# Kernel optimization log

Measured on AMD Instinct MI355X. Metric: run time of the kernel, lower is better.

The kernel has to match this reference:

```python
import jax, jax.numpy as jnp
import numpy as np

D = 1024
H = 16
HD = D // H  # 64
FF = 4 * D
EPS = 1e-5


def _xavier(key, shape):
    fan_in, fan_out = shape[1], shape[0]
    limit = float(np.sqrt(6.0 / (fan_in + fan_out)))
    return jax.random.uniform(key, shape, jnp.float32, -limit, limit)


def setup_inputs() -> dict:
    key = jax.random.key(0)
    ks = jax.random.split(key, 8)
    x = jax.random.normal(ks[0], (2, 2048, D), jnp.float32)
    return {
        "x": x,
        "w_qkv": _xavier(ks[1], (3 * D, D)),
        "b_qkv": jnp.zeros((3 * D,), jnp.float32),
        "w_out": _xavier(ks[2], (D, D)),
        "b_out": jnp.zeros((D,), jnp.float32),
        "w1": _xavier(ks[3], (FF, D)),
        "b1": jnp.zeros((FF,), jnp.float32),
        "w2": _xavier(ks[4], (D, FF)),
        "b2": jnp.zeros((D,), jnp.float32),
        "ln1_g": jnp.ones((D,), jnp.float32),
        "ln1_b": jnp.zeros((D,), jnp.float32),
        "ln2_g": jnp.ones((D,), jnp.float32),
        "ln2_b": jnp.zeros((D,), jnp.float32),
    }


def _layernorm(x, g, b):
    mu = jnp.mean(x, -1, keepdims=True)
    var = jnp.mean(jnp.square(x - mu), -1, keepdims=True)
    return (x - mu) * jax.lax.rsqrt(var + EPS) * g + b


def reference(x, w_qkv, b_qkv, w_out, b_out, w1, b1, w2, b2,
              ln1_g, ln1_b, ln2_g, ln2_b):
    B, S, _ = x.shape
    # pre-LN attention branch
    h = _layernorm(x, ln1_g, ln1_b)
    qkv = h @ w_qkv.T + b_qkv                      # [B,S,3D]
    qkv = qkv.reshape(B, S, H, 3 * HD).transpose(0, 2, 1, 3)  # [B,H,S,3hd]
    q, k, v = jnp.split(qkv, 3, axis=-1)
    scores = jnp.einsum('bhqd,bhkd->bhqk', q, k) / np.sqrt(HD)
    attn = jax.nn.softmax(scores, axis=-1)
    ctx = jnp.einsum('bhqk,bhkd->bhqd', attn, v)   # [B,H,S,hd]
    ctx = ctx.transpose(0, 2, 1, 3).reshape(B, S, D)
    x = x + (ctx @ w_out.T + b_out)
    # pre-LN MLP branch
    h = _layernorm(x, ln2_g, ln2_b)
    h = jax.nn.relu(h @ w1.T + b1)
    x = x + (h @ w2.T + b2)
    return x
```

## Files before the change

kernel.cpp:

```cpp
#include <hip/hip_runtime.h>
#include <hip/hip_bf16.h>

typedef __attribute__((ext_vector_type(8))) short bf16x8;
typedef __attribute__((ext_vector_type(4))) float f32x4;
typedef __attribute__((ext_vector_type(16))) float f32x16;
typedef __attribute__((ext_vector_type(4))) unsigned short u16x4;
typedef __attribute__((ext_vector_type(4))) unsigned int u32x4;
typedef unsigned short u16;

__device__ __forceinline__ u16 f2bf(float f) {
  unsigned u = __builtin_bit_cast(unsigned, f);
  u += 0x7fffu + ((u >> 16) & 1u);
  return (u16)(u >> 16);
}
__device__ __forceinline__ float bf2f(u16 u) {
  unsigned v = ((unsigned)u) << 16;
  return __builtin_bit_cast(float, v);
}
__device__ __forceinline__ unsigned cvt_pk_bf16(float lo, float hi) {
  unsigned r;
  asm("v_cvt_pk_bf16_f32 %0, %1, %2" : "=v"(r) : "v"(lo), "v"(hi));
  return r;
}
__device__ __forceinline__ float exp2_fast(float x) {
  float r;
  asm("v_exp_f32 %0, %1" : "=v"(r) : "v"(x));
  return r;
}

__device__ __forceinline__ void gl_lds16(const void* g, void* l) {
  __builtin_amdgcn_global_load_lds((const __attribute__((address_space(1))) void*)g,
                                   (__attribute__((address_space(3))) void*)l,
                                   16, 0, 0);
}

__device__ __forceinline__ void bar() {
  asm volatile("" ::: "memory");
  __builtin_amdgcn_s_barrier();
  asm volatile("" ::: "memory");
}

__global__ __launch_bounds__(256) void ln_cvt(const float* __restrict__ x,
                                              const float* __restrict__ g,
                                              const float* __restrict__ b,
                                              u16* __restrict__ out,
                                              const float* __restrict__ wa,
                                              const float* __restrict__ wb,
                                              const float* __restrict__ wc,
                                              const float* __restrict__ wd,
                                              u16* __restrict__ oa,
                                              u16* __restrict__ ob,
                                              u16* __restrict__ oc,
                                              u16* __restrict__ od) {
  __shared__ float red[8];
  const int t = threadIdx.x;
  if (blockIdx.x < 4096) {
    const int row = blockIdx.x;
    const int lane = t & 63, w = t >> 6;
    const float4 v = ((const float4*)(x + (size_t)row * 1024))[t];
    float s = v.x + v.y + v.z + v.w;
    float q = v.x * v.x + v.y * v.y + v.z * v.z + v.w * v.w;
#pragma unroll
    for (int off = 32; off; off >>= 1) {
      s += __shfl_down(s, off);
      q += __shfl_down(q, off);
    }
    if (lane == 0) { red[w] = s; red[4 + w] = q; }
    __syncthreads();
    s = red[0] + red[1] + red[2] + red[3];
    q = red[4] + red[5] + red[6] + red[7];
    const float mu = s * (1.f / 1024.f);
    const float var = q * (1.f / 1024.f) - mu * mu;
    const float rs = rsqrtf(var + 1e-5f);
    const float4 gv = ((const float4*)g)[t];
    const float4 bv = ((const float4*)b)[t];
    u16x4 o;
    o.x = f2bf((v.x - mu) * rs * gv.x + bv.x);
    o.y = f2bf((v.y - mu) * rs * gv.y + bv.y);
    o.z = f2bf((v.z - mu) * rs * gv.z + bv.z);
    o.w = f2bf((v.w - mu) * rs * gv.w + bv.w);
    ((u16x4*)(out + (size_t)row * 1024))[t] = o;
  } else {
    int i = (blockIdx.x - 4096) * 256 + t;
    const int stride = 2048 * 256;
    for (; i < 3145728; i += stride) {
      const float* src;
      u16* dst;
      int j;
      if (i < 786432) { src = wa; dst = oa; j = i; }
      else if (i < 1048576) { src = wb; dst = ob; j = i - 786432; }
      else if (i < 2097152) { src = wc; dst = oc; j = i - 1048576; }
      else { src = wd; dst = od; j = i - 2097152; }
      float4 v = ((const float4*)src)[j];
      u16x4 o;
      o.x = f2bf(v.x); o.y = f2bf(v.y); o.z = f2bf(v.z); o.w = f2bf(v.w);
      ((u16x4*)dst)[j] = o;
    }
  }
}

__global__ __launch_bounds__(256) void ln_k(const float* __restrict__ x,
                                            const float* __restrict__ g,
                                            const float* __restrict__ b,
                                            u16* __restrict__ out) {
  const int row = blockIdx.x;
  const int t = threadIdx.x;
  const int lane = t & 63, w = t >> 6;
  const float4 v = ((const float4*)(x + (size_t)row * 1024))[t];
  float s = v.x + v.y + v.z + v.w;
  float q = v.x * v.x + v.y * v.y + v.z * v.z + v.w * v.w;
#pragma unroll
  for (int off = 32; off; off >>= 1) {
    s += __shfl_down(s, off);
    q += __shfl_down(q, off);
  }
  __shared__ float red[8];
  if (lane == 0) { red[w] = s; red[4 + w] = q; }
  __syncthreads();
  s = red[0] + red[1] + red[2] + red[3];
  q = red[4] + red[5] + red[6] + red[7];
  const float mu = s * (1.f / 1024.f);
  const float var = q * (1.f / 1024.f) - mu * mu;
  const float rs = rsqrtf(var + 1e-5f);
  const float4 gv = ((const float4*)g)[t];
  const float4 bv = ((const float4*)b)[t];
  u16x4 o;
  o.x = f2bf((v.x - mu) * rs * gv.x + bv.x);
  o.y = f2bf((v.y - mu) * rs * gv.y + bv.y);
  o.z = f2bf((v.z - mu) * rs * gv.z + bv.z);
  o.w = f2bf((v.w - mu) * rs * gv.w + bv.w);
  ((u16x4*)(out + (size_t)row * 1024))[t] = o;
}

template <int EPI>
__global__ __launch_bounds__(512, 2) void gemm8(const u16* __restrict__ A,
                                                const u16* __restrict__ B,
                                                const float* __restrict__ bias,
                                                void* __restrict__ outp,
                                                const int N, const int K) {
  __shared__ u16 lds[65536];
  const int t = threadIdx.x;
  const int lane = t & 63, w = t >> 6;
  const int wm = w >> 2, wn = w & 3;
  const int l15 = lane & 15, lhi = lane >> 4;
  const int nbx = gridDim.x;
  const int nwg = nbx * gridDim.y;
  const int orig = blockIdx.y * nbx + blockIdx.x;
  const int cpx = nwg >> 3;
  const int lid = (orig & 7) * cpx + (orig >> 3);
  const long bm = (long)(lid / nbx) * 256, bn = (long)(lid % nbx) * 256;
  const u16* Ab = A + bm * K;
  const u16* Bb = B + bn * K;
  const int nt = K >> 6;
  const int ni2 = nt >> 1;

  const int srow0 = t >> 3, sg0 = (t & 7) ^ (srow0 & 7);
  const int srow1 = 64 + srow0, sg1 = (t & 7) ^ (srow1 & 7);

#define STAGE8(Mb, hf, kt_, dstb)                                             \
  do {                                                                        \
    const long kk_ = (long)(kt_) << 6;                                        \
    gl_lds16(Mb + (size_t)((hf) * 128 + srow0) * K + kk_ + sg0 * 8,           \
             &lds[(dstb) + w * 512]);                                         \
    gl_lds16(Mb + (size_t)((hf) * 128 + srow1) * K + kk_ + sg1 * 8,           \
             &lds[(dstb) + 4096 + w * 512]);                                  \
  } while (0)

#define LOADA(db, mi, fk0, fk1)                                               \
  {                                                                           \
    const int r_ = (mi) * 16 + l15;                                           \
    const int b_ = ((db) * 2 + wm) * 8192 + r_ * 64;                          \
    fk0 = *(const bf16x8*)&lds[b_ + ((lhi ^ (r_ & 7)) << 3)];                 \
    fk1 = *(const bf16x8*)&lds[b_ + (((4 + lhi) ^ (r_ & 7)) << 3)];           \
  }

#define LOADB(db)                                                             \
  _Pragma("unroll")                                                           \
  for (int ni = 0; ni < 4; ++ni) {                                            \
    const int R_ = wn * 64 + ni * 16 + l15;                                   \
    const int b_ = 32768 + ((db) * 2 + (R_ >> 7)) * 8192 + (R_ & 127) * 64;   \
    bq[ni][0] = *(const bf16x8*)&lds[b_ + ((lhi ^ (R_ & 7)) << 3)];           \
    bq[ni][1] = *(const bf16x8*)&lds[b_ + (((4 + lhi) ^ (R_ & 7)) << 3)];     \
  }

#define MM(q, a0k0, a0k1, a1k0, a1k1)                                         \
  __builtin_amdgcn_s_setprio(1);                                              \
  _Pragma("unroll")                                                           \
  for (int ni = 0; ni < 4; ++ni) {                                            \
    acc[2 * (q)][ni] = __builtin_amdgcn_mfma_f32_16x16x32_bf16(               \
        a0k0, bq[ni][0], acc[2 * (q)][ni], 0, 0, 0);                          \
    acc[2 * (q)][ni] = __builtin_amdgcn_mfma_f32_16x16x32_bf16(               \
        a0k1, bq[ni][1], acc[2 * (q)][ni], 0, 0, 0);                          \
    acc[2 * (q) + 1][ni] = __builtin_amdgcn_mfma_f32_16x16x32_bf16(           \
        a1k0, bq[ni][0], acc[2 * (q) + 1][ni], 0, 0, 0);                      \
    acc[2 * (q) + 1][ni] = __builtin_amdgcn_mfma_f32_16x16x32_bf16(           \
        a1k1, bq[ni][1], acc[2 * (q) + 1][ni], 0, 0, 0);                      \
  }                                                                           \
  __builtin_amdgcn_s_setprio(0);

  f32x4 acc[8][4] = {};
  STAGE8(Bb, 0, 0, 32768 + 0);
  STAGE8(Bb, 1, 0, 32768 + 8192);
  STAGE8(Ab, 0, 0, 0);
  STAGE8(Ab, 1, 0, 8192);
  STAGE8(Bb, 0, 1, 32768 + 16384);
  STAGE8(Bb, 1, 1, 32768 + 24576);
  asm volatile("s_waitcnt vmcnt(4)" ::: "memory");
  bar();

  for (int it = 0; it < ni2; ++it) {
    const int t0 = 2 * it, t1 = 2 * it + 1;
    const bool sN = (it + 1) < ni2;
    bf16x8 bq[4][2];
    bf16x8 a0, a1, a2, a3;
    LOADA(0, 0, a0, a1) LOADA(0, 1, a2, a3) LOADB(0);
    STAGE8(Ab, 0, t1, 16384);
    bar();
    MM(0, a0, a1, a2, a3)
    bar();
    LOADA(0, 2, a0, a1) LOADA(0, 3, a2, a3)
    STAGE8(Ab, 1, t1, 24576);
    if (sN) STAGE8(Bb, 0, t0 + 2, 32768 + 0);
    bar();
    MM(1, a0, a1, a2, a3)
    bar();
    LOADA(0, 4, a0, a1) LOADA(0, 5, a2, a3)
    if (sN) STAGE8(Bb, 1, t0 + 2, 32768 + 8192);
    bar();
    MM(2, a0, a1, a2, a3)
    bar();
    LOADA(0, 6, a0, a1) LOADA(0, 7, a2, a3)
    if (sN) asm volatile("s_waitcnt vmcnt(4)" ::: "memory");
    else    asm volatile("s_waitcnt vmcnt(0)" ::: "memory");
    bar();
    MM(3, a0, a1, a2, a3)
    bar();
    LOADA(1, 0, a0, a1) LOADA(1, 1, a2, a3) LOADB(1);
    if (sN) STAGE8(Ab, 0, t0 + 2, 0);
    bar();
    MM(0, a0, a1, a2, a3)
    bar();
    LOADA(1, 2, a0, a1) LOADA(1, 3, a2, a3)
    if (sN) {
      STAGE8(Ab, 1, t0 + 2, 8192);
      STAGE8(Bb, 0, t1 + 2, 32768 + 16384);
    }
    bar();
    MM(1, a0, a1, a2, a3)
    bar();
    LOADA(1, 4, a0, a1) LOADA(1, 5, a2, a3)
    if (sN) STAGE8(Bb, 1, t1 + 2, 32768 + 24576);
    bar();
    MM(2, a0, a1, a2, a3)
    bar();
    LOADA(1, 6, a0, a1) LOADA(1, 7, a2, a3)
    if (sN) asm volatile("s_waitcnt vmcnt(4)" ::: "memory");
    else    asm volatile("s_waitcnt vmcnt(0)" ::: "memory");
    bar();
    MM(3, a0, a1, a2, a3)
    bar();
  }
#undef STAGE8
#undef LOADA
#undef LOADB
#undef MM
#pragma unroll
  for (int ni = 0; ni < 4; ++ni) {
    const long col = bn + wn * 64 + ni * 16 + l15;
    const float bj = bias[col];
#pragma unroll
    for (int mi = 0; mi < 8; ++mi) {
      const long row0 = bm + wm * 128 + mi * 16 + lhi * 4;
#pragma unroll
      for (int r = 0; r < 4; ++r) {
        const float v = acc[mi][ni][r] + bj;
        const long idx = (row0 + r) * N + col;
        if constexpr (EPI == 0) {
          ((u16*)outp)[idx] = f2bf(v);
        } else {
          ((u16*)outp)[idx] = f2bf(v > 0.f ? v : 0.f);
        }
      }
    }
  }
}

template <int BM, int BN, int BK, int TH, int WN, int MR, int NR, int EPI>
__global__ __launch_bounds__(TH, 2) void gemm_rot(const u16* __restrict__ A,
                                                  const u16* __restrict__ B,
                                                  const float* __restrict__ bias,
                                                  const float* __restrict__ res,
                                                  void* __restrict__ outp,
                                                  const int N, const int K) {
  constexpr int GPR = BK / 8;
  constexpr int KS = BK / 32;
  constexpr int AELEMS = BM * BK;
  constexpr int BELEMS = BN * BK;
  constexpr int NC = (BM + BN) * GPR / TH;
  static_assert((BM * GPR) % TH == 0 && ((BM + BN) * GPR) % TH == 0, "");
  __shared__ u16 lds[3][AELEMS + BELEMS];
  const int t = threadIdx.x;
  const int lane = t & 63, w = t >> 6;
  const int wm = w / WN, wn = w % WN;
  const int l15 = lane & 15, lhi = lane >> 4;
  const int nbx = gridDim.x;
  const int nwg = nbx * gridDim.y;
  const int orig = blockIdx.y * nbx + blockIdx.x;
  const int cpx = nwg >> 3;
  const int lid = (orig & 7) * cpx + (orig >> 3);
  const long bm = (long)(lid / nbx) * BM, bn = (long)(lid % nbx) * BN;
  const u16* Ab = A + bm * K;
  const u16* Bb = B + bn * K;
  const int nk = K / BK;

#define STAGE(kt_, bufi)                                                      \
  do {                                                                        \
    const long kk_ = (long)(kt_) * BK;                                        \
    _Pragma("unroll")                                                         \
    for (int j = 0; j < NC; ++j) {                                            \
      const int sj = j * TH + t;                                              \
      const u16* src_;                                                        \
      if ((j + 1) * TH <= BM * GPR) {                                         \
        const int row_ = sj / GPR, grp_ = sj % GPR;                           \
        const int g_ = (BK == 32) ? (grp_ ^ ((row_ >> 1) & 3))                \
                                  : (grp_ ^ (row_ & 7));                      \
        src_ = Ab + (size_t)row_ * K + kk_ + g_ * 8;                          \
      } else {                                                                \
        const int sb_ = sj - BM * GPR;                                        \
        const int row_ = sb_ / GPR, grp_ = sb_ % GPR;                         \
        const int g_ = (BK == 32) ? (grp_ ^ ((row_ >> 1) & 3))                \
                                  : (grp_ ^ (row_ & 7));                      \
        src_ = Bb + (size_t)row_ * K + kk_ + g_ * 8;                          \
      }                                                                       \
      gl_lds16(src_, &lds[bufi][(size_t)(j * TH + w * 64) * 8]);              \
    }                                                                         \
  } while (0)

  f32x4 acc[MR][NR] = {};
  STAGE(0, 0);
  STAGE(1, 1);
  for (int i = 0; i < nk; ++i) {
    if (i + 1 < nk) {
      if constexpr (NC == 3)      asm volatile("s_waitcnt vmcnt(3)" ::: "memory");
      else if constexpr (NC == 4) asm volatile("s_waitcnt vmcnt(4)" ::: "memory");
      else                        asm volatile("s_waitcnt vmcnt(6)" ::: "memory");
    } else {
      asm volatile("s_waitcnt vmcnt(0)" ::: "memory");
    }
    bar();
    if (i + 2 < nk) STAGE(i + 2, (i + 2) % 3);
    const u16* bufA = lds[i % 3];
    const u16* bufB = bufA + AELEMS;
    bf16x8 av[MR][KS], bv[NR][KS];
#pragma unroll
    for (int ii = 0; ii < MR; ++ii) {
      const int R = wm * (MR * 16) + ii * 16 + l15;
#pragma unroll
      for (int ks = 0; ks < KS; ++ks) {
        const int pos = (BK == 32) ? (lhi ^ ((R >> 1) & 3))
                                   : ((ks * 4 + lhi) ^ (R & 7));
        av[ii][ks] = *(const bf16x8*)&bufA[R * BK + (pos << 3)];
      }
    }
#pragma unroll
    for (int jj = 0; jj < NR; ++jj) {
      const int R = wn * (NR * 16) + jj * 16 + l15;
#pragma unroll
      for (int ks = 0; ks < KS; ++ks) {
        const int pos = (BK == 32) ? (lhi ^ ((R >> 1) & 3))
                                   : ((ks * 4 + lhi) ^ (R & 7));
        bv[jj][ks] = *(const bf16x8*)&bufB[R * BK + (pos << 3)];
      }
    }
    __builtin_amdgcn_s_setprio(1);
#pragma unroll
    for (int ii = 0; ii < MR; ++ii)
#pragma unroll
      for (int jj = 0; jj < NR; ++jj)
#pragma unroll
        for (int ks = 0; ks < KS; ++ks)
          acc[ii][jj] = __builtin_amdgcn_mfma_f32_16x16x32_bf16(av[ii][ks], bv[jj][ks],
                                                                acc[ii][jj], 0, 0, 0);
    __builtin_amdgcn_s_setprio(0);
  }
#undef STAGE
#pragma unroll
  for (int jj = 0; jj < NR; ++jj) {
    const long col = bn + wn * (NR * 16) + jj * 16 + l15;
    const float bj = bias[col];
#pragma unroll
    for (int ii = 0; ii < MR; ++ii) {
      const long row0 = bm + wm * (MR * 16) + ii * 16 + lhi * 4;
#pragma unroll
      for (int r = 0; r < 4; ++r) {
        const float v = acc[ii][jj][r] + bj;
        const long idx = (row0 + r) * N + col;
        if constexpr (EPI == 0) {
          ((u16*)outp)[idx] = f2bf(v);
        } else if constexpr (EPI == 1) {
          ((float*)outp)[idx] = v + res[idx];
        } else {
          ((u16*)outp)[idx] = f2bf(v > 0.f ? v : 0.f);
        }
      }
    }
  }
}

__global__ __launch_bounds__(256) void vtrans(const u16* __restrict__ qkv,
                                              u16* __restrict__ vt) {
  const int t = threadIdx.x;
  const int bh = blockIdx.y, b = bh >> 4, h = bh & 15;
  const int kvb = blockIdx.x * 64;
  __shared__ u16 tile[64][72];
  const u16* src = qkv + ((size_t)(b * 2048 + kvb)) * 3072 + h * 192 + 128;
#pragma unroll
  for (int rr = 0; rr < 2; ++rr) {
    const int e = rr * 2048 + t * 8;
    const int kv = e >> 6, d = e & 63;
    *(bf16x8*)&tile[kv][d] = *(const bf16x8*)(src + (size_t)kv * 3072 + d);
  }
  __syncthreads();
#pragma unroll
  for (int rr = 0; rr < 2; ++rr) {
    const int e = rr * 2048 + t * 8;
    const int d = e >> 6, kv = e & 63;
    bf16x8 o;
#pragma unroll
    for (int j = 0; j < 8; ++j) o[j] = (short)tile[kv + j][d];
    *(bf16x8*)(vt + ((size_t)bh * 64 + d) * 2048 + kvb + kv) = o;
  }
}

__global__ __launch_bounds__(256, 4) void attn_k(const u16* __restrict__ qkv,
                                                 const u16* __restrict__ vt,
                                                 u16* __restrict__ part0,
                                                 u16* __restrict__ part1,
                                                 float* __restrict__ lbuf) {
  __shared__ u16 kt[2][4096];
  __shared__ u16 vtl[2][4096];
  const int t = threadIdx.x;
  const int lane = t & 63, w = t >> 6;
  const int l31 = lane & 31, hl = lane >> 5;
  const int l7 = l31 & 7;
  const int lid = blockIdx.x + 16 * blockIdx.y + 512 * blockIdx.z;
  const int bh = (lid & 7) * 4 + ((lid >> 3) & 3);
  const int qblk = (lid >> 5) & 15;
  const int sidx = lid >> 9;
  const int b = bh >> 4, h = bh & 15;
  const int qb = qblk * 128 + w * 32;
  const int kvbeg = sidx * 1024, kvend = kvbeg + 1024;

  const float qscale = 0.125f * 1.44269504f;
  const u16* qp = qkv + ((size_t)(b * 2048 + qb + l31)) * 3072 + h * 192;
  bf16x8 qf[4];
#pragma unroll
  for (int ds = 0; ds < 4; ++ds) {
    bf16x8 v = *(const bf16x8*)(qp + 16 * ds + 8 * hl);
#pragma unroll
    for (int j = 0; j < 8; ++j) v[j] = (short)f2bf(bf2f((u16)v[j]) * qscale);
    qf[ds] = v;
  }
  bf16x8 ones;
#pragma unroll
  for (int j = 0; j < 8; ++j) ones[j] = (short)0x3F80;

  const int srow = t >> 3, sgc = t & 7;
  const int sswz = (sgc ^ (srow & 7)) * 8;
  const u16* kg0 = qkv + ((size_t)(b * 2048 + srow)) * 3072 + h * 192 + 64 + sswz;
  const u16* vg0 = vt + (size_t)bh * 64 * 2048 + (size_t)srow * 2048 + sswz;

  f32x16 o0 = {}, o1 = {}, ol = {};

#define STAGE(bufi, kv0i)                                              \
  do {                                                                 \
    const u16* ks_ = kg0 + (size_t)(kv0i) * 3072;                      \
    const u16* vs_ = vg0 + (kv0i);                                     \
    gl_lds16(ks_, &kt[bufi][w * 512]);                                 \
    gl_lds16(ks_ + (size_t)32 * 3072, &kt[bufi][2048 + w * 512]);      \
    gl_lds16(vs_, &vtl[bufi][w * 512]);                                \
    gl_lds16(vs_ + (size_t)32 * 2048, &vtl[bufi][2048 + w * 512]);     \
  } while (0)

#define PACK(dst, SA, tl)                                                 \
  do {                                                                    \
    unsigned A0 = cvt_pk_bf16(SA[8 * tl + 0], SA[8 * tl + 1]);            \
    unsigned A1 = cvt_pk_bf16(SA[8 * tl + 2], SA[8 * tl + 3]);            \
    unsigned B0 = cvt_pk_bf16(SA[8 * tl + 4], SA[8 * tl + 5]);            \
    unsigned B1 = cvt_pk_bf16(SA[8 * tl + 6], SA[8 * tl + 7]);            \
    asm volatile("v_permlane32_swap_b32 %0, %1" : "+v"(A0), "+v"(B0));    \
    asm volatile("v_permlane32_swap_b32 %0, %1" : "+v"(A1), "+v"(B1));    \
    u32x4 pv_ = {A0, A1, B0, B1};                                         \
    dst = __builtin_bit_cast(bf16x8, pv_);                                \
  } while (0)

  int buf = 0;
  STAGE(0, kvbeg);
  for (int kv0 = kvbeg; kv0 < kvend; kv0 += 64) {
    asm volatile("s_waitcnt vmcnt(0)" ::: "memory");
    bar();
    if (kv0 + 64 < kvend) STAGE(buf ^ 1, kv0 + 64);
    f32x16 sa0 = {}, sa1 = {};
    __builtin_amdgcn_s_setprio(1);
#pragma unroll
    for (int ds = 0; ds < 4; ++ds) {
      const bf16x8 kf0 = *(const bf16x8*)&kt[buf][l31 * 64 + (((2 * ds + hl) ^ l7) << 3)];
      const bf16x8 kf1 = *(const bf16x8*)&kt[buf][(32 + l31) * 64 + (((2 * ds + hl) ^ l7) << 3)];
      sa0 = __builtin_amdgcn_mfma_f32_32x32x16_bf16(kf0, qf[ds], sa0, 0, 0, 0);
      sa1 = __builtin_amdgcn_mfma_f32_32x32x16_bf16(kf1, qf[ds], sa1, 0, 0, 0);
    }
    __builtin_amdgcn_s_setprio(0);
#pragma unroll
    for (int i = 0; i < 16; ++i) sa0[i] = exp2_fast(sa0[i]);
#pragma unroll
    for (int i = 0; i < 16; ++i) sa1[i] = exp2_fast(sa1[i]);
    bf16x8 pf0, pf1, pf2, pf3;
    PACK(pf0, sa0, 0);
    PACK(pf1, sa0, 1);
    PACK(pf2, sa1, 0);
    PACK(pf3, sa1, 1);
    __builtin_amdgcn_s_setprio(1);
#pragma unroll
    for (int t4i = 0; t4i < 4; ++t4i) {
      const bf16x8 vf0 = *(const bf16x8*)&vtl[buf][l31 * 64 + (((2 * t4i + hl) ^ l7) << 3)];
      const bf16x8 vf1 = *(const bf16x8*)&vtl[buf][(32 + l31) * 64 + (((2 * t4i + hl) ^ l7) << 3)];
      const bf16x8 pf = (t4i == 0) ? pf0 : (t4i == 1) ? pf1 : (t4i == 2) ? pf2 : pf3;
      o0 = __builtin_amdgcn_mfma_f32_32x32x16_bf16(vf0, pf, o0, 0, 0, 0);
      o1 = __builtin_amdgcn_mfma_f32_32x32x16_bf16(vf1, pf, o1, 0, 0, 0);
      ol = __builtin_amdgcn_mfma_f32_32x32x16_bf16(ones, pf, ol, 0, 0, 0);
    }
    __builtin_amdgcn_s_setprio(0);
    buf ^= 1;
  }
#undef STAGE
#undef PACK
  bar();
  if (lane < 32) {
    lbuf[(size_t)(sidx * 32 + bh) * 2048 + qb + l31] = ol[0];
  }
  u16* obase = (sidx == 0) ? part0 : part1;
  u16* ow = ((u16*)kt) + w * 2048;
#pragma unroll
  for (int g2 = 0; g2 < 4; ++g2) {
    uint2 v0, v1;
    v0.x = cvt_pk_bf16(o0[4 * g2 + 0], o0[4 * g2 + 1]);
    v0.y = cvt_pk_bf16(o0[4 * g2 + 2], o0[4 * g2 + 3]);
    v1.x = cvt_pk_bf16(o1[4 * g2 + 0], o1[4 * g2 + 1]);
    v1.y = cvt_pk_bf16(o1[4 * g2 + 2], o1[4 * g2 + 3]);
    *(uint2*)&ow[l31 * 64 + ((g2 ^ l7) << 3) + hl * 4] = v0;
    *(uint2*)&ow[l31 * 64 + (((4 + g2) ^ l7) << 3) + hl * 4] = v1;
  }
#pragma unroll
  for (int p = 0; p < 4; ++p) {
    const int q = 8 * p + (lane >> 3);
    const int gpos = lane & 7;
    const bf16x8 val = *(const bf16x8*)&ow[q * 64 + (gpos << 3)];
    const int gd = gpos ^ (q & 7);
    *(bf16x8*)(obase + ((size_t)(b * 2048 + qb + q)) * 1024 + h * 64 + gd * 8) = val;
  }
}

__global__ __launch_bounds__(256) void attn_merge(const u16* __restrict__ p1,
                                                  const float* __restrict__ lbuf,
                                                  u16* __restrict__ ctx) {
  const int c = blockIdx.x * 256 + threadIdx.x;
  const int row = c >> 7;
  const int b = row >> 11, q = row & 2047;
  const int h = (c >> 3) & 15;
  const int bh = b * 16 + h;
  const float l1 = lbuf[(size_t)bh * 2048 + q];
  const float l2 = lbuf[(size_t)(32 + bh) * 2048 + q];
  const float inv = 1.f / (l1 + l2);
  const bf16x8 v0 = ((const bf16x8*)ctx)[c];
  const bf16x8 v1 = ((const bf16x8*)p1)[c];
  float r[8];
#pragma unroll
  for (int j = 0; j < 8; ++j)
    r[j] = (bf2f((u16)v0[j]) + bf2f((u16)v1[j])) * inv;
  u32x4 ov = {cvt_pk_bf16(r[0], r[1]), cvt_pk_bf16(r[2], r[3]),
              cvt_pk_bf16(r[4], r[5]), cvt_pk_bf16(r[6], r[7])};
  ((u32x4*)ctx)[c] = ov;
}

extern "C" void kernel_launch(void* const* d_in, const int* in_sizes, int n_in,
                              void* d_out, int out_size, void* d_ws, size_t ws_size,
                              hipStream_t stream) {
  const float* x     = (const float*)d_in[0];
  const float* w_qkv = (const float*)d_in[1];
  const float* b_qkv = (const float*)d_in[2];
  const float* w_out = (const float*)d_in[3];
  const float* b_out = (const float*)d_in[4];
  const float* w1    = (const float*)d_in[5];
  const float* b1    = (const float*)d_in[6];
  const float* w2    = (const float*)d_in[7];
  const float* b2    = (const float*)d_in[8];
  const float* ln1g  = (const float*)d_in[9];
  const float* ln1b  = (const float*)d_in[10];
  const float* ln2g  = (const float*)d_in[11];
  const float* ln2b  = (const float*)d_in[12];
  float* out = (float*)d_out;

  u16* wqkv_b = (u16*)d_ws;
  u16* wout_b = wqkv_b + (size_t)3072 * 1024;
  u16* w1_b   = wout_b + (size_t)1024 * 1024;
  u16* w2_b   = w1_b + (size_t)4096 * 1024;
  u16* r1     = w2_b + (size_t)1024 * 4096;
  u16* r2     = r1 + (size_t)4096 * 1024;
  u16* qkvb   = r2;
  u16* vtb    = r2 + (size_t)4096 * 3072;
  float* x2   = (float*)(r2 + (size_t)4096 * 4096);
  u16* part1  = (u16*)x2;
  float* lbuf = (float*)(part1 + (size_t)4096 * 1024);

  ln_cvt<<<6144, 256, 0, stream>>>(x, ln1g, ln1b, r1,
                                   w_qkv, w_out, w1, w2,
                                   wqkv_b, wout_b, w1_b, w2_b);

  gemm8<0><<<dim3(12, 16), 512, 0, stream>>>(r1, wqkv_b, b_qkv, qkvb, 3072, 1024);
  vtrans<<<dim3(32, 32), 256, 0, stream>>>(qkvb, vtb);
  attn_k<<<dim3(16, 32, 2), 256, 0, stream>>>(qkvb, vtb, r1, part1, lbuf);
  attn_merge<<<2048, 256, 0, stream>>>(part1, lbuf, r1);
  gemm_rot<64, 128, 64, 256, 2, 2, 4, 1><<<dim3(8, 64), 256, 0, stream>>>(
      r1, wout_b, b_out, x, x2, 1024, 1024);
  ln_k<<<4096, 256, 0, stream>>>(x2, ln2g, ln2b, r1);
  gemm8<2><<<dim3(16, 16), 512, 0, stream>>>(r1, w1_b, b1, r2, 4096, 1024);
  gemm_rot<64, 128, 64, 256, 2, 2, 4, 1><<<dim3(8, 64), 256, 0, stream>>>(
      r2, w2_b, b2, x2, out, 1024, 4096);
}
```

Before: 212.1 us.

## Software-pipeline PV MFMA one step behind QK and drop ones-MFMA row sum

Restructures the attention inner loop so the P·V MFMAs for the previous KV tile run right after the current Q·K MFMAs, overlapping them with the exp/pack VALU work. V gets a triple-buffered LDS region to match. The softmax denominator is now summed in VALU with a cross-half shuffle instead of an extra MFMA against a ones vector. This cuts matrix-core work by a third in the PV stage, but adds LDS use and VALU reductions that may lower occupancy. The row sum also now comes from fp32 probabilities rather than the bf16-rounded ones used in PV.

```diff
diff --git a/kernel.cpp b/kernel.cpp
--- a/kernel.cpp
+++ b/kernel.cpp
@@ -438,7 +438,7 @@
                                                  u16* __restrict__ part1,
                                                  float* __restrict__ lbuf) {
   __shared__ u16 kt[2][4096];
-  __shared__ u16 vtl[2][4096];
+  __shared__ u16 vtl[3][4096];
   const int t = threadIdx.x;
   const int lane = t & 63, w = t >> 6;
   const int l31 = lane & 31, hl = lane >> 5;
@@ -449,7 +449,7 @@
   const int sidx = lid >> 9;
   const int b = bh >> 4, h = bh & 15;
   const int qb = qblk * 128 + w * 32;
-  const int kvbeg = sidx * 1024, kvend = kvbeg + 1024;
+  const int kvbeg = sidx * 1024;
 
   const float qscale = 0.125f * 1.44269504f;
   const u16* qp = qkv + ((size_t)(b * 2048 + qb + l31)) * 3072 + h * 192;
@@ -461,25 +461,24 @@
     for (int j = 0; j < 8; ++j) v[j] = (short)f2bf(bf2f((u16)v[j]) * qscale);
     qf[ds] = v;
   }
-  bf16x8 ones;
-#pragma unroll
-  for (int j = 0; j < 8; ++j) ones[j] = (short)0x3F80;
 
   const int srow = t >> 3, sgc = t & 7;
   const int sswz = (sgc ^ (srow & 7)) * 8;
   const u16* kg0 = qkv + ((size_t)(b * 2048 + srow)) * 3072 + h * 192 + 64 + sswz;
   const u16* vg0 = vt + (size_t)bh * 64 * 2048 + (size_t)srow * 2048 + sswz;
 
-  f32x16 o0 = {}, o1 = {}, ol = {};
-
-#define STAGE(bufi, kv0i)                                              \
+  f32x16 o0 = {}, o1 = {};
+  float lsum = 0.f;
+  bf16x8 pfp0, pfp1, pfp2, pfp3;
+
+#define STAGE(kb, vb, kv0i)                                            \
   do {                                                                 \
     const u16* ks_ = kg0 + (size_t)(kv0i) * 3072;                      \
     const u16* vs_ = vg0 + (kv0i);                                     \
-    gl_lds16(ks_, &kt[bufi][w * 512]);                                 \
-    gl_lds16(ks_ + (size_t)32 * 3072, &kt[bufi][2048 + w * 512]);      \
-    gl_lds16(vs_, &vtl[bufi][w * 512]);                                \
-    gl_lds16(vs_ + (size_t)32 * 2048, &vtl[bufi][2048 + w * 512]);     \
+    gl_lds16(ks_, &kt[kb][w * 512]);                                   \
+    gl_lds16(ks_ + (size_t)32 * 3072, &kt[kb][2048 + w * 512]);        \
+    gl_lds16(vs_, &vtl[vb][w * 512]);                                  \
+    gl_lds16(vs_ + (size_t)32 * 2048, &vtl[vb][2048 + w * 512]);       \
   } while (0)
 
 #define PACK(dst, SA, tl)                                                 \
@@ -494,49 +493,69 @@
     dst = __builtin_bit_cast(bf16x8, pv_);                                \
   } while (0)
 
-  int buf = 0;
-  STAGE(0, kvbeg);
-  for (int kv0 = kvbeg; kv0 < kvend; kv0 += 64) {
+#define PVSTEP(vbuf)                                                          \
+  do {                                                                        \
+    __builtin_amdgcn_s_setprio(1);                                            \
+    _Pragma("unroll")                                                         \
+    for (int t4i = 0; t4i < 4; ++t4i) {                                       \
+      const bf16x8 vf0 = *(const bf16x8*)&(vbuf)[l31 * 64 + (((2 * t4i + hl) ^ l7) << 3)]; \
+      const bf16x8 vf1 = *(const bf16x8*)&(vbuf)[(32 + l31) * 64 + (((2 * t4i + hl) ^ l7) << 3)]; \
+      const bf16x8 pf = (t4i == 0) ? pfp0 : (t4i == 1) ? pfp1                 \
+                       : (t4i == 2) ? pfp2 : pfp3;                            \
+      o0 = __builtin_amdgcn_mfma_f32_32x32x16_bf16(vf0, pf, o0, 0, 0, 0);     \
+      o1 = __builtin_amdgcn_mfma_f32_32x32x16_bf16(vf1, pf, o1, 0, 0, 0);     \
+    }                                                                         \
+    __builtin_amdgcn_s_setprio(0);                                            \
+  } while (0)
+
+  STAGE(0, 0, kvbeg);
+  for (int it = 0; it < 16; ++it) {
     asm volatile("s_waitcnt vmcnt(0)" ::: "memory");
     bar();
-    if (kv0 + 64 < kvend) STAGE(buf ^ 1, kv0 + 64);
+    if (it + 1 < 16) STAGE((it + 1) & 1, (it + 1) % 3, kvbeg + (it + 1) * 64);
+    const u16* kbuf = &kt[it & 1][0];
     f32x16 sa0 = {}, sa1 = {};
     __builtin_amdgcn_s_setprio(1);
 #pragma unroll
     for (int ds = 0; ds < 4; ++ds) {
-      const bf16x8 kf0 = *(const bf16x8*)&kt[buf][l31 * 64 + (((2 * ds + hl) ^ l7) << 3)];
-      const bf16x8 kf1 = *(const bf16x8*)&kt[buf][(32 + l31) * 64 + (((2 * ds + hl) ^ l7) << 3)];
+      const bf16x8 kf0 = *(const bf16x8*)&kbuf[l31 * 64 + (((2 * ds + hl) ^ l7) << 3)];
+      const bf16x8 kf1 = *(const bf16x8*)&kbuf[(32 + l31) * 64 + (((2 * ds + hl) ^ l7) << 3)];
       sa0 = __builtin_amdgcn_mfma_f32_32x32x16_bf16(kf0, qf[ds], sa0, 0, 0, 0);
       sa1 = __builtin_amdgcn_mfma_f32_32x32x16_bf16(kf1, qf[ds], sa1, 0, 0, 0);
     }
     __builtin_amdgcn_s_setprio(0);
+    if (it > 0) {
+      const u16* vprev = &vtl[(it - 1) % 3][0];
+      PVSTEP(vprev);
+    }
 #pragma unroll
     for (int i = 0; i < 16; ++i) sa0[i] = exp2_fast(sa0[i]);
 #pragma unroll
     for (int i = 0; i < 16; ++i) sa1[i] = exp2_fast(sa1[i]);
-    bf16x8 pf0, pf1, pf2, pf3;
-    PACK(pf0, sa0, 0);
-    PACK(pf1, sa0, 1);
-    PACK(pf2, sa1, 0);
-    PACK(pf3, sa1, 1);
-    __builtin_amdgcn_s_setprio(1);
-#pragma unroll
-    for (int t4i = 0; t4i < 4; ++t4i) {
-      const bf16x8 vf0 = *(const bf16x8*)&vtl[buf][l31 * 64 + (((2 * t4i + hl) ^ l7) << 3)];
-      const bf16x8 vf1 = *(const bf16x8*)&vtl[buf][(32 + l31) * 64 + (((2 * t4i + hl) ^ l7) << 3)];
-      const bf16x8 pf = (t4i == 0) ? pf0 : (t4i == 1) ? pf1 : (t4i == 2) ? pf2 : pf3;
-      o0 = __builtin_amdgcn_mfma_f32_32x32x16_bf16(vf0, pf, o0, 0, 0, 0);
-      o1 = __builtin_amdgcn_mfma_f32_32x32x16_bf16(vf1, pf, o1, 0, 0, 0);
-      ol = __builtin_amdgcn_mfma_f32_32x32x16_bf16(ones, pf, ol, 0, 0, 0);
-    }
-    __builtin_amdgcn_s_setprio(0);
-    buf ^= 1;
+    const f32x16 ps = sa0 + sa1;
+    float s8[8];
+#pragma unroll
+    for (int i = 0; i < 8; ++i) s8[i] = ps[i] + ps[i + 8];
+    const float q0s = (s8[0] + s8[1]) + (s8[2] + s8[3]);
+    const float q1s = (s8[4] + s8[5]) + (s8[6] + s8[7]);
+    float rsum = q0s + q1s;
+    rsum += __shfl_xor(rsum, 32);
+    lsum += rsum;
+    PACK(pfp0, sa0, 0);
+    PACK(pfp1, sa0, 1);
+    PACK(pfp2, sa1, 0);
+    PACK(pfp3, sa1, 1);
+  }
+  {
+    const u16* vprev = &vtl[15 % 3][0];
+    PVSTEP(vprev);
   }
 #undef STAGE
 #undef PACK
+#undef PVSTEP
   bar();
   if (lane < 32) {
-    lbuf[(size_t)(sidx * 32 + bh) * 2048 + qb + l31] = ol[0];
+    lbuf[(size_t)(sidx * 32 + bh) * 2048 + qb + l31] = lsum;
   }
   u16* obase = (sidx == 0) ? part0 : part1;
   u16* ow = ((u16*)kt) + w * 2048;
```

Result: no change. 211.7 us (-0.2%).

## Double attention block size and replace ones-MFMA row sum with VALU reduction

Applied to the files above, without the earlier changes.

The attention kernel now runs 512-thread blocks covering 256 queries, so each staged 64-row K/V tile is shared by eight waves instead of four. Each thread now issues one K load and one V load per stage, where before it issued two of each. The softmax denominator is no longer built by a third MFMA against a ones vector. It is summed on the VALU from the fp32 exponentials, with a cross-half lane shuffle. The trade-off is fewer blocks and heavier per-block register and LDS pressure, and the row sum now uses unrounded values rather than the bf16 P.

```diff
diff --git a/kernel.cpp b/kernel.cpp
--- a/kernel.cpp
+++ b/kernel.cpp
@@ -432,24 +432,23 @@
   }
 }
 
-__global__ __launch_bounds__(256, 4) void attn_k(const u16* __restrict__ qkv,
+__global__ __launch_bounds__(512, 4) void attn_k(const u16* __restrict__ qkv,
                                                  const u16* __restrict__ vt,
                                                  u16* __restrict__ part0,
                                                  u16* __restrict__ part1,
                                                  float* __restrict__ lbuf) {
-  __shared__ u16 kt[2][4096];
-  __shared__ u16 vtl[2][4096];
+  __shared__ u16 smem[16384];
   const int t = threadIdx.x;
   const int lane = t & 63, w = t >> 6;
   const int l31 = lane & 31, hl = lane >> 5;
   const int l7 = l31 & 7;
-  const int lid = blockIdx.x + 16 * blockIdx.y + 512 * blockIdx.z;
+  const int lid = blockIdx.x + 8 * blockIdx.y + 256 * blockIdx.z;
   const int bh = (lid & 7) * 4 + ((lid >> 3) & 3);
-  const int qblk = (lid >> 5) & 15;
-  const int sidx = lid >> 9;
+  const int qblk = (lid >> 5) & 7;
+  const int sidx = lid >> 8;
   const int b = bh >> 4, h = bh & 15;
-  const int qb = qblk * 128 + w * 32;
-  const int kvbeg = sidx * 1024, kvend = kvbeg + 1024;
+  const int qb = qblk * 256 + w * 32;
+  const int kvbeg = sidx * 1024;
 
   const float qscale = 0.125f * 1.44269504f;
   const u16* qp = qkv + ((size_t)(b * 2048 + qb + l31)) * 3072 + h * 192;
@@ -461,25 +460,19 @@
     for (int j = 0; j < 8; ++j) v[j] = (short)f2bf(bf2f((u16)v[j]) * qscale);
     qf[ds] = v;
   }
-  bf16x8 ones;
-#pragma unroll
-  for (int j = 0; j < 8; ++j) ones[j] = (short)0x3F80;
 
   const int srow = t >> 3, sgc = t & 7;
   const int sswz = (sgc ^ (srow & 7)) * 8;
   const u16* kg0 = qkv + ((size_t)(b * 2048 + srow)) * 3072 + h * 192 + 64 + sswz;
   const u16* vg0 = vt + (size_t)bh * 64 * 2048 + (size_t)srow * 2048 + sswz;
 
-  f32x16 o0 = {}, o1 = {}, ol = {};
+  f32x16 o0 = {}, o1 = {};
+  float lsum = 0.f;
 
 #define STAGE(bufi, kv0i)                                              \
   do {                                                                 \
-    const u16* ks_ = kg0 + (size_t)(kv0i) * 3072;                      \
-    const u16* vs_ = vg0 + (kv0i);                                     \
-    gl_lds16(ks_, &kt[bufi][w * 512]);                                 \
-    gl_lds16(ks_ + (size_t)32 * 3072, &kt[bufi][2048 + w * 512]);      \
-    gl_lds16(vs_, &vtl[bufi][w * 512]);                                \
-    gl_lds16(vs_ + (size_t)32 * 2048, &vtl[bufi][2048 + w * 512]);     \
+    gl_lds16(kg0 + (size_t)(kv0i) * 3072, &smem[(bufi) * 4096 + w * 512]); \
+    gl_lds16(vg0 + (kv0i), &smem[8192 + (bufi) * 4096 + w * 512]);     \
   } while (0)
 
 #define PACK(dst, SA, tl)                                                 \
@@ -496,16 +489,18 @@
 
   int buf = 0;
   STAGE(0, kvbeg);
-  for (int kv0 = kvbeg; kv0 < kvend; kv0 += 64) {
+  for (int it = 0; it < 16; ++it) {
     asm volatile("s_waitcnt vmcnt(0)" ::: "memory");
     bar();
-    if (kv0 + 64 < kvend) STAGE(buf ^ 1, kv0 + 64);
+    if (it + 1 < 16) STAGE(buf ^ 1, kvbeg + (it + 1) * 64);
+    const u16* kbuf = &smem[buf * 4096];
+    const u16* vbuf = &smem[8192 + buf * 4096];
     f32x16 sa0 = {}, sa1 = {};
     __builtin_amdgcn_s_setprio(1);
 #pragma unroll
     for (int ds = 0; ds < 4; ++ds) {
-      const bf16x8 kf0 = *(const bf16x8*)&kt[buf][l31 * 64 + (((2 * ds + hl) ^ l7) << 3)];
-      const bf16x8 kf1 = *(const bf16x8*)&kt[buf][(32 + l31) * 64 + (((2 * ds + hl) ^ l7) << 3)];
+      const bf16x8 kf0 = *(const bf16x8*)&kbuf[l31 * 64 + (((2 * ds + hl) ^ l7) << 3)];
+      const bf16x8 kf1 = *(const bf16x8*)&kbuf[(32 + l31) * 64 + (((2 * ds + hl) ^ l7) << 3)];
       sa0 = __builtin_amdgcn_mfma_f32_32x32x16_bf16(kf0, qf[ds], sa0, 0, 0, 0);
       sa1 = __builtin_amdgcn_mfma_f32_32x32x16_bf16(kf1, qf[ds], sa1, 0, 0, 0);
     }
@@ -514,6 +509,15 @@
     for (int i = 0; i < 16; ++i) sa0[i] = exp2_fast(sa0[i]);
 #pragma unroll
     for (int i = 0; i < 16; ++i) sa1[i] = exp2_fast(sa1[i]);
+    const f32x16 ps = sa0 + sa1;
+    float s8[8];
+#pragma unroll
+    for (int i = 0; i < 8; ++i) s8[i] = ps[i] + ps[i + 8];
+    const float q0s = (s8[0] + s8[1]) + (s8[2] + s8[3]);
+    const float q1s = (s8[4] + s8[5]) + (s8[6] + s8[7]);
+    float rsum = q0s + q1s;
+    rsum += __shfl_xor(rsum, 32);
+    lsum += rsum;
     bf16x8 pf0, pf1, pf2, pf3;
     PACK(pf0, sa0, 0);
     PACK(pf1, sa0, 1);
@@ -522,12 +526,11 @@
     __builtin_amdgcn_s_setprio(1);
 #pragma unroll
     for (int t4i = 0; t4i < 4; ++t4i) {
-      const bf16x8 vf0 = *(const bf16x8*)&vtl[buf][l31 * 64 + (((2 * t4i + hl) ^ l7) << 3)];
-      const bf16x8 vf1 = *(const bf16x8*)&vtl[buf][(32 + l31) * 64 + (((2 * t4i + hl) ^ l7) << 3)];
+      const bf16x8 vf0 = *(const bf16x8*)&vbuf[l31 * 64 + (((2 * t4i + hl) ^ l7) << 3)];
+      const bf16x8 vf1 = *(const bf16x8*)&vbuf[(32 + l31) * 64 + (((2 * t4i + hl) ^ l7) << 3)];
       const bf16x8 pf = (t4i == 0) ? pf0 : (t4i == 1) ? pf1 : (t4i == 2) ? pf2 : pf3;
       o0 = __builtin_amdgcn_mfma_f32_32x32x16_bf16(vf0, pf, o0, 0, 0, 0);
       o1 = __builtin_amdgcn_mfma_f32_32x32x16_bf16(vf1, pf, o1, 0, 0, 0);
-      ol = __builtin_amdgcn_mfma_f32_32x32x16_bf16(ones, pf, ol, 0, 0, 0);
     }
     __builtin_amdgcn_s_setprio(0);
     buf ^= 1;
@@ -536,10 +539,10 @@
 #undef PACK
   bar();
   if (lane < 32) {
-    lbuf[(size_t)(sidx * 32 + bh) * 2048 + qb + l31] = ol[0];
+    lbuf[(size_t)(sidx * 32 + bh) * 2048 + qb + l31] = lsum;
   }
   u16* obase = (sidx == 0) ? part0 : part1;
-  u16* ow = ((u16*)kt) + w * 2048;
+  u16* ow = &smem[w * 2048];
 #pragma unroll
   for (int g2 = 0; g2 < 4; ++g2) {
     uint2 v0, v1;
@@ -618,7 +621,7 @@
 
   gemm8<0><<<dim3(12, 16), 512, 0, stream>>>(r1, wqkv_b, b_qkv, qkvb, 3072, 1024);
   vtrans<<<dim3(32, 32), 256, 0, stream>>>(qkvb, vtb);
-  attn_k<<<dim3(16, 32, 2), 256, 0, stream>>>(qkvb, vtb, r1, part1, lbuf);
+  attn_k<<<dim3(8, 32, 2), 512, 0, stream>>>(qkvb, vtb, r1, part1, lbuf);
   attn_merge<<<2048, 256, 0, stream>>>(part1, lbuf, r1);
   gemm_rot<64, 128, 64, 256, 2, 2, 4, 1><<<dim3(8, 64), 256, 0, stream>>>(
       r1, wout_b, b_out, x, x2, 1024, 1024);
```

Result: no change. 209.5 us (-1.2%).
